# Kernel tuning notes

Hardware: AMD Instinct MI355X
Metric: run time of the kernel (lower is better)

The kernel has to match this reference:

```python
import jax, jax.numpy as jnp
import numpy as np

B, S_IN, S_CTX = 2, 4096, 512
INPUT_DIM = CTX_DIM = DIM = 1024
NUM_HEADS = 16
HEAD_DIM = DIM // NUM_HEADS
BASE = 10000.0


def rms_norm(x, scale, eps=1e-6):
    xf = x.astype(jnp.float32)
    rrms = jax.lax.rsqrt(jnp.mean(xf * xf, axis=-1, keepdims=True) + eps)
    return (xf * rrms).astype(x.dtype) * scale


def apply_rope(x, pos):
    # x: [B, N, H, D]; rotate-half RoPE over full head_dim
    d = x.shape[-1]
    inv_freq = 1.0 / (BASE ** (jnp.arange(0, d, 2, dtype=jnp.float32) / d))  # [d/2]
    ang = pos.astype(jnp.float32)[:, None] * inv_freq[None, :]  # [N, d/2]
    cos = jnp.cos(ang)[None, :, None, :]
    sin = jnp.sin(ang)[None, :, None, :]
    x1, x2 = x[..., : d // 2], x[..., d // 2 :]
    return jnp.concatenate([x1 * cos - x2 * sin, x2 * cos + x1 * sin], axis=-1).astype(x.dtype)


def setup_inputs() -> dict:
    key = jax.random.key(0)
    ks = jax.random.split(key, 8)
    std = 0.02
    return {
        "input": jax.random.normal(ks[0], (B, S_IN, INPUT_DIM), jnp.float32),
        "context": jax.random.normal(ks[1], (B, S_CTX, CTX_DIM), jnp.float32),
        "W_qkv_in": jax.random.normal(ks[2], (3 * DIM, INPUT_DIM), jnp.float32) * std,
        "b_qkv_in": jnp.zeros((3 * DIM,), jnp.float32),
        "W_qkv_ctx": jax.random.normal(ks[3], (3 * DIM, CTX_DIM), jnp.float32) * std,
        "b_qkv_ctx": jnp.zeros((3 * DIM,), jnp.float32),
        "q_scale_in": jnp.ones((DIM,), jnp.float32),
        "k_scale_in": jnp.ones((DIM,), jnp.float32),
        "q_scale_ctx": jnp.ones((DIM,), jnp.float32),
        "k_scale_ctx": jnp.ones((DIM,), jnp.float32),
        "W_out_in": jax.random.normal(ks[4], (INPUT_DIM, DIM), jnp.float32) * std,
        "b_out_in": jnp.zeros((INPUT_DIM,), jnp.float32),
        "W_out_ctx": jax.random.normal(ks[5], (CTX_DIM, DIM), jnp.float32) * std,
        "b_out_ctx": jnp.zeros((CTX_DIM,), jnp.float32),
    }


def reference(input, context, W_qkv_in, b_qkv_in, W_qkv_ctx, b_qkv_ctx,
              q_scale_in, k_scale_in, q_scale_ctx, k_scale_ctx,
              W_out_in, b_out_in, W_out_ctx, b_out_ctx):
    # dual-stream QKV projections
    qkv_i = input @ W_qkv_in.T + b_qkv_in        # [B, S_in, 3*DIM]
    qkv_c = context @ W_qkv_ctx.T + b_qkv_ctx    # [B, S_ctx, 3*DIM]
    qi, ki, vi = jnp.split(qkv_i, 3, axis=-1)
    qc, kc, vc = jnp.split(qkv_c, 3, axis=-1)
    # QK-RMSNorm over full dim (as in QKNorm(dim))
    qi, ki = rms_norm(qi, q_scale_in), rms_norm(ki, k_scale_in)
    qc, kc = rms_norm(qc, q_scale_ctx), rms_norm(kc, k_scale_ctx)
    # concat context first, then input
    q = jnp.concatenate([qc, qi], axis=1)  # [B, N, DIM]
    k = jnp.concatenate([kc, ki], axis=1)
    v = jnp.concatenate([vc, vi], axis=1)
    N = q.shape[1]
    pos = jnp.arange(N)
    # RoPE applied per head
    q = apply_rope(q.reshape(B, N, NUM_HEADS, HEAD_DIM), pos).reshape(B, N, DIM)
    k = apply_rope(k.reshape(B, N, NUM_HEADS, HEAD_DIM), pos).reshape(B, N, DIM)
    # single-head attention over full dim (faithful to source: heads flattened before q@k^T)
    scale = HEAD_DIM ** -0.5
    attn = jax.nn.softmax(jnp.einsum('bnd,bmd->bnm', q, k) * scale, axis=-1)
    out = jnp.einsum('bnm,bmd->bnd', attn, v)  # [B, N, DIM]
    s_ctx = context.shape[1]
    input_output = out[:, s_ctx:, :] @ W_out_in.T + b_out_in
    context_output = out[:, :s_ctx, :] @ W_out_ctx.T + b_out_ctx
    return (input_output, context_output)
```

## Files before the change

### kernel.cpp

```cpp
#include <hip/hip_runtime.h>
#include <stdint.h>

typedef unsigned short u16;
typedef __bf16 bf16x8 __attribute__((ext_vector_type(8)));
typedef float f32x4 __attribute__((ext_vector_type(4)));

typedef const __attribute__((address_space(1))) uint32_t* gu32p;
typedef __attribute__((address_space(3))) uint32_t* lu32p;
#define GLOAD_LDS16(g, l) \
  __builtin_amdgcn_global_load_lds((gu32p)(const void*)(g), (lu32p)(void*)(l), 16, 0, 0)

static __device__ __forceinline__ u16 f2bf(float f) {
  uint32_t u = __builtin_bit_cast(uint32_t, f);
  return (u16)((u + 0x7FFFu + ((u >> 16) & 1u)) >> 16);
}
static __device__ __forceinline__ float bf2f(u16 h) {
  uint32_t u = ((uint32_t)h) << 16;
  return __builtin_bit_cast(float, u);
}

__global__ __launch_bounds__(256) void k_conv_all(
    const float* __restrict__ s0, u16* __restrict__ d0,
    const float* __restrict__ s1, u16* __restrict__ d1,
    const float* __restrict__ s2, u16* __restrict__ d2,
    const float* __restrict__ s3, u16* __restrict__ d3,
    const float* __restrict__ s4, u16* __restrict__ d4,
    const float* __restrict__ s5, u16* __restrict__ d5) {
  int b = blockIdx.x;
  const float* src; u16* dst; long off;
  if (b < 8192)       { src = s0; dst = d0; off = (long)b * 1024; }
  else if (b < 9216)  { src = s1; dst = d1; off = (long)(b - 8192) * 1024; }
  else if (b < 12288) { src = s2; dst = d2; off = (long)(b - 9216) * 1024; }
  else if (b < 15360) { src = s3; dst = d3; off = (long)(b - 12288) * 1024; }
  else if (b < 16384) { src = s4; dst = d4; off = (long)(b - 15360) * 1024; }
  else                { src = s5; dst = d5; off = (long)(b - 16384) * 1024; }
  long i = off + threadIdx.x * 4;
  const float4 v = *(const float4*)&src[i];
  ushort4 o;
  o.x = f2bf(v.x); o.y = f2bf(v.y); o.z = f2bf(v.z); o.w = f2bf(v.w);
  *(ushort4*)&dst[i] = o;
}

__device__ __forceinline__ void gemm_bk64(const u16* __restrict__ A, const u16* __restrict__ Bt,
                                          int lda, int ldb, long row0, long col0,
                                          int kbeg, int kend, u16* smem, f32x4 acc[4][4]) {
  const int tid = threadIdx.x;
  const int l = tid & 63;
  const int w = tid >> 6;
  const int wm = w >> 1, wn = w & 1;
  const int lr = l & 15, kg = l >> 4;
  const int swz = (lr & 7) * 8;
  const int r_l = tid >> 3;
  const int ssrc = ((tid & 7) ^ (r_l & 7)) * 8;
  const u16* gA = &A[(row0 + r_l) * (long)lda + ssrc];
  const u16* gB = &Bt[(col0 + r_l) * (long)ldb + ssrc];
  u16* const ldsA = smem + w * 512;
  u16* const ldsB = smem + 8192 + w * 512;
  const int NT = (kend - kbeg) >> 6;

  {
#pragma unroll
    for (int c = 0; c < 4; ++c) {
      GLOAD_LDS16(gA + (c * 32) * (long)lda + kbeg, ldsA + c * 2048);
      GLOAD_LDS16(gB + (c * 32) * (long)ldb + kbeg, ldsB + c * 2048);
    }
  }
  asm volatile("s_waitcnt vmcnt(0)" ::: "memory");
  __builtin_amdgcn_s_barrier();
  __builtin_amdgcn_sched_barrier(0);

  for (int t = 0; t < NT; ++t) {
    const int d = (t & 1) << 14;
    const int dn = ((t + 1) & 1) << 14;
    const bool pf = (t + 1 < NT);
    const long k1 = kbeg + (long)(t + 1) * 64;
    bf16x8 af[4], bv[4];
    if (pf) {
#pragma unroll
      for (int c = 0; c < 4; ++c)
        GLOAD_LDS16(gA + (c * 32) * (long)lda + k1, ldsA + dn + c * 2048);
    }
#pragma unroll
    for (int i = 0; i < 4; ++i) {
      af[i] = *(const bf16x8*)&smem[d + (wm * 64 + i * 16 + lr) * 64 + (kg * 8 ^ swz)];
      bv[i] = *(const bf16x8*)&smem[d + 8192 + (wn * 64 + i * 16 + lr) * 64 + (kg * 8 ^ swz)];
    }
    __builtin_amdgcn_s_setprio(1);
#pragma unroll
    for (int mf = 0; mf < 4; ++mf)
#pragma unroll
      for (int nf = 0; nf < 4; ++nf)
        acc[mf][nf] = __builtin_amdgcn_mfma_f32_16x16x32_bf16(af[mf], bv[nf], acc[mf][nf], 0, 0, 0);
    __builtin_amdgcn_s_setprio(0);
    if (pf) {
#pragma unroll
      for (int c = 0; c < 4; ++c)
        GLOAD_LDS16(gB + (c * 32) * (long)ldb + k1, ldsB + dn + c * 2048);
    }
#pragma unroll
    for (int i = 0; i < 4; ++i) {
      af[i] = *(const bf16x8*)&smem[d + (wm * 64 + i * 16 + lr) * 64 + ((32 + kg * 8) ^ swz)];
      bv[i] = *(const bf16x8*)&smem[d + 8192 + (wn * 64 + i * 16 + lr) * 64 + ((32 + kg * 8) ^ swz)];
    }
    __builtin_amdgcn_s_setprio(1);
#pragma unroll
    for (int mf = 0; mf < 4; ++mf)
#pragma unroll
      for (int nf = 0; nf < 4; ++nf)
        acc[mf][nf] = __builtin_amdgcn_mfma_f32_16x16x32_bf16(af[mf], bv[nf], acc[mf][nf], 0, 0, 0);
    __builtin_amdgcn_s_setprio(0);
    asm volatile("s_waitcnt vmcnt(0)" ::: "memory");
    __builtin_amdgcn_s_barrier();
    __builtin_amdgcn_sched_barrier(0);
  }
}

#define EPI_VARS                                   \
  const int l = threadIdx.x & 63;                  \
  const int w = threadIdx.x >> 6;                  \
  const int wm = w >> 1, wn = w & 1;               \
  const int mrow = (l >> 4) * 4, ncol = l & 15;

__global__ __launch_bounds__(256, 2) void k_gemm_qkv(
    const u16* __restrict__ XIN, const u16* __restrict__ XCTX,
    const u16* __restrict__ WQI, const u16* __restrict__ WQC,
    const float* __restrict__ bqi, const float* __restrict__ bqc,
    u16* __restrict__ qb, u16* __restrict__ kb, u16* __restrict__ vt) {
  __shared__ u16 smem[32768];
  f32x4 acc[4][4] = {};
  const bool isCtx = blockIdx.x >= 64;
  const u16* X = isCtx ? XCTX : XIN;
  const u16* W = isCtx ? WQC : WQI;
  const float* bias = isCtx ? bqc : bqi;
  const int seg_start = isCtx ? 0 : 512;
  long row0 = (long)(isCtx ? blockIdx.x - 64 : blockIdx.x) * 128;
  long col0 = (long)blockIdx.y * 128;
  gemm_bk64(X, W, 1024, 1024, row0, col0, 0, 1024, smem, acc);
  EPI_VARS
#pragma unroll
  for (int mf = 0; mf < 4; ++mf)
#pragma unroll
    for (int nf = 0; nf < 4; ++nf)
#pragma unroll
      for (int r = 0; r < 4; ++r) {
        int m = (int)row0 + wm * 64 + mf * 16 + mrow + r;
        int n = (int)col0 + wn * 64 + nf * 16 + ncol;
        float v = acc[mf][nf][r] + bias[n];
        int b, s;
        if (isCtx) { b = m >> 9; s = m & 511; } else { b = m >> 12; s = m & 4095; }
        long grow = (long)b * 4608 + seg_start + s;
        if (n < 1024)      qb[grow * 1024 + n] = f2bf(v);
        else if (n < 2048) kb[grow * 1024 + (n - 1024)] = f2bf(v);
        else               vt[((long)b * 1024 + (n - 2048)) * 4608 + seg_start + s] = f2bf(v);
      }
}

__global__ __launch_bounds__(256) void k_normrope(u16* __restrict__ qb, u16* __restrict__ kb,
                                                  const float* __restrict__ qsi, const float* __restrict__ ksi,
                                                  const float* __restrict__ qsc, const float* __restrict__ ksc) {
  __shared__ float sm[4];
  const int row = blockIdx.x;
  const int which = blockIdx.y;
  const int n = row % 4608;
  u16* buf = which ? kb : qb;
  const float* scale = which ? (n < 512 ? ksc : ksi) : (n < 512 ? qsc : qsi);
  u16* rp = buf + (long)row * 1024;
  const int t = threadIdx.x;
  const int h = t >> 4;
  const int jj = (t & 15) * 2;
  const int e1 = h * 64 + jj;
  const int e2 = e1 + 32;
  uint32_t u1 = *(const uint32_t*)&rp[e1];
  uint32_t u2 = *(const uint32_t*)&rp[e2];
  float x1a = bf2f((u16)u1), x1b = bf2f((u16)(u1 >> 16));
  float x2a = bf2f((u16)u2), x2b = bf2f((u16)(u2 >> 16));
  float ss = x1a * x1a + x1b * x1b + x2a * x2a + x2b * x2b;
#pragma unroll
  for (int o = 32; o; o >>= 1) ss += __shfl_xor(ss, o, 64);
  if ((t & 63) == 0) sm[t >> 6] = ss;
  __syncthreads();
  ss = sm[0] + sm[1] + sm[2] + sm[3];
  const float rr = rsqrtf(ss * (1.0f / 1024.0f) + 1e-6f);
  float s1a = scale[e1], s1b = scale[e1 + 1], s2a = scale[e2], s2b = scale[e2 + 1];
  x1a *= rr * s1a; x1b *= rr * s1b; x2a *= rr * s2a; x2b *= rr * s2b;
  const float c = -13.287712379549449f / 32.0f;
  float fa = exp2f((float)jj * c), fb = exp2f((float)(jj + 1) * c);
  float sna, csa, snb, csb;
  sincosf((float)n * fa, &sna, &csa);
  sincosf((float)n * fb, &snb, &csb);
  u16 o1a = f2bf(x1a * csa - x2a * sna), o1b = f2bf(x1b * csb - x2b * snb);
  u16 o2a = f2bf(x2a * csa + x1a * sna), o2b = f2bf(x2b * csb + x1b * snb);
  *(uint32_t*)&rp[e1] = (uint32_t)o1a | ((uint32_t)o1b << 16);
  *(uint32_t*)&rp[e2] = (uint32_t)o2a | ((uint32_t)o2b << 16);
}

__global__ __launch_bounds__(256, 2) void k_gemm_p(const u16* __restrict__ Q, const u16* __restrict__ Kb,
                                                   u16* __restrict__ P) {
  __shared__ u16 smem[32768];
  f32x4 acc[4][4] = {};
  long row0 = (long)blockIdx.x * 128;
  long col0 = (long)blockIdx.y * 128;
  gemm_bk64(Q, Kb, 1024, 1024, row0, col0, 0, 1024, smem, acc);
  EPI_VARS
#pragma unroll
  for (int mf = 0; mf < 4; ++mf)
#pragma unroll
    for (int nf = 0; nf < 4; ++nf)
#pragma unroll
      for (int r = 0; r < 4; ++r) {
        long m = row0 + wm * 64 + mf * 16 + mrow + r;
        long n = col0 + wn * 64 + nf * 16 + ncol;
        P[m * 4608 + n] = f2bf(__expf(acc[mf][nf][r] * 0.125f));
      }
}

__global__ __launch_bounds__(256) void k_rowsum(const u16* __restrict__ P, float* __restrict__ RS) {
  __shared__ float sm[4];
  const long row = blockIdx.x;
  const uint32_t* pr = (const uint32_t*)(P + row * 4608);
  const int t = threadIdx.x;
  float s = 0.f;
#pragma unroll
  for (int i = 0; i < 9; ++i) {
    uint32_t u = pr[i * 256 + t];
    s += bf2f((u16)u) + bf2f((u16)(u >> 16));
  }
#pragma unroll
  for (int o = 32; o; o >>= 1) s += __shfl_xor(s, o, 64);
  if ((t & 63) == 0) sm[t >> 6] = s;
  __syncthreads();
  if (t == 0) RS[row] = sm[0] + sm[1] + sm[2] + sm[3];
}

__global__ __launch_bounds__(256, 2) void k_gemm_o(const u16* __restrict__ P, const u16* __restrict__ VT,
                                                   float* __restrict__ OP) {
  __shared__ u16 smem[32768];
  f32x4 acc[4][4] = {};
  long row0 = (long)blockIdx.x * 128;
  long col0 = (long)blockIdx.y * 128;
  const int kc = blockIdx.z;
  gemm_bk64(P, VT, 4608, 4608, row0, col0, kc * 2304, (kc + 1) * 2304, smem, acc);
  float* op = OP + (long)kc * 4608 * 1024;
  EPI_VARS
#pragma unroll
  for (int mf = 0; mf < 4; ++mf)
#pragma unroll
    for (int nf = 0; nf < 4; ++nf)
#pragma unroll
      for (int r = 0; r < 4; ++r) {
        long m = row0 + wm * 64 + mf * 16 + mrow + r;
        long n = col0 + wn * 64 + nf * 16 + ncol;
        op[m * 1024 + n] = acc[mf][nf][r];
      }
}

__global__ __launch_bounds__(256) void k_reduce2div(const float* __restrict__ OP,
                                                    const float* __restrict__ RS,
                                                    u16* __restrict__ AO) {
  const long st = 4608L * 1024;
  long i = ((long)blockIdx.x * 256 + threadIdx.x) * 4;
  const float inv = 1.0f / RS[i >> 10];
  float4 a = *(const float4*)&OP[i];
  float4 b = *(const float4*)&OP[i + st];
  ushort4 o;
  o.x = f2bf((a.x + b.x) * inv);
  o.y = f2bf((a.y + b.y) * inv);
  o.z = f2bf((a.z + b.z) * inv);
  o.w = f2bf((a.w + b.w) * inv);
  *(ushort4*)&AO[i] = o;
}

__global__ __launch_bounds__(256, 2) void k_gemm_out2(const u16* __restrict__ AO,
                                                      const u16* __restrict__ WOI, const u16* __restrict__ WOC,
                                                      const float* __restrict__ boi, const float* __restrict__ boc,
                                                      float* __restrict__ out) {
  __shared__ u16 smem[32768];
  f32x4 acc[4][4] = {};
  long row0 = (long)blockIdx.x * 128;
  long col0 = (long)blockIdx.y * 128;
  int b = (int)(row0 / 4608);
  int s0 = (int)(row0 % 4608);
  const bool ctx = s0 < 512;
  const u16* W = ctx ? WOC : WOI;
  const float* bias = ctx ? boc : boi;
  float* ob = ctx ? out + 8388608 + ((long)b * 512 + s0) * 1024
                  : out + ((long)b * 4096 + (s0 - 512)) * 1024;
  gemm_bk64(AO, W, 1024, 1024, row0, col0, 0, 1024, smem, acc);
  EPI_VARS
#pragma unroll
  for (int mf = 0; mf < 4; ++mf)
#pragma unroll
    for (int nf = 0; nf < 4; ++nf)
#pragma unroll
      for (int r = 0; r < 4; ++r) {
        long m = wm * 64 + mf * 16 + mrow + r;
        long n = col0 + wn * 64 + nf * 16 + ncol;
        ob[m * 1024 + n] = acc[mf][nf][r] + bias[n];
      }
}

extern "C" void kernel_launch(void* const* d_in, const int* in_sizes, int n_in,
                              void* d_out, int out_size, void* d_ws, size_t ws_size,
                              hipStream_t stream) {
  const float* input   = (const float*)d_in[0];
  const float* context = (const float*)d_in[1];
  const float* Wqi     = (const float*)d_in[2];
  const float* bqi     = (const float*)d_in[3];
  const float* Wqc     = (const float*)d_in[4];
  const float* bqc     = (const float*)d_in[5];
  const float* qsi     = (const float*)d_in[6];
  const float* ksi     = (const float*)d_in[7];
  const float* qsc     = (const float*)d_in[8];
  const float* ksc     = (const float*)d_in[9];
  const float* Woi     = (const float*)d_in[10];
  const float* boi     = (const float*)d_in[11];
  const float* Woc     = (const float*)d_in[12];
  const float* boc     = (const float*)d_in[13];
  float* out = (float*)d_out;

  uint8_t* ws = (uint8_t*)d_ws;
  u16* XIN  = (u16*)(ws + 0);
  u16* XCTX = (u16*)(ws + 16777216);
  u16* WQI  = (u16*)(ws + 18874368);
  u16* WQC  = (u16*)(ws + 25165824);
  u16* WOI  = (u16*)(ws + 31457280);
  u16* WOC  = (u16*)(ws + 33554432);
  u16* QB   = (u16*)(ws + 35651584);
  u16* KB   = (u16*)(ws + 54525952);
  u16* VT   = (u16*)(ws + 73400320);
  u16* AO   = (u16*)(ws + 92274688);
  float* S32 = (float*)(ws + 111149056);
  float* RS  = (float*)(ws + 186646528);
  u16* PB   = (u16*)(ws + 196083712);

  k_conv_all<<<dim3(17408), 256, 0, stream>>>(input, XIN, context, XCTX, Wqi, WQI,
                                              Wqc, WQC, Woi, WOI, Woc, WOC);

  k_gemm_qkv<<<dim3(72, 24), 256, 0, stream>>>(XIN, XCTX, WQI, WQC, bqi, bqc, QB, KB, VT);

  k_normrope<<<dim3(9216, 2), 256, 0, stream>>>(QB, KB, qsi, ksi, qsc, ksc);

  for (int b = 0; b < 2; ++b) {
    const u16* Qb  = QB + (long)b * 4608 * 1024;
    const u16* Kbp = KB + (long)b * 4608 * 1024;
    const u16* VTb = VT + (long)b * 1024 * 4608;
    u16* AOb = AO + (long)b * 4608 * 1024;
    k_gemm_p<<<dim3(36, 36), 256, 0, stream>>>(Qb, Kbp, PB);
    k_rowsum<<<dim3(4608), 256, 0, stream>>>(PB, RS);
    k_gemm_o<<<dim3(36, 8, 2), 256, 0, stream>>>(PB, VTb, (float*)S32);
    k_reduce2div<<<dim3(4608), 256, 0, stream>>>((const float*)S32, RS, AOb);
  }

  k_gemm_out2<<<dim3(72, 8), 256, 0, stream>>>(AO, WOI, WOC, boi, boc, out);
}
```

Baseline: 442.1 us.

## Use single-buffered high-occupancy GEMM for scores and split PV into three K-chunks

```diff
diff --git a/kernel.cpp b/kernel.cpp
--- a/kernel.cpp
+++ b/kernel.cpp
@@ -115,6 +115,48 @@
   }
 }
 
+__device__ __forceinline__ void gemm_sb64(const u16* __restrict__ A, const u16* __restrict__ Bt,
+                                          int lda, int ldb, long row0, long col0,
+                                          int kbeg, int kend, u16* smem, f32x4 acc[4][4]) {
+  const int tid = threadIdx.x;
+  const int l = tid & 63;
+  const int w = tid >> 6;
+  const int wm = w >> 1, wn = w & 1;
+  const int lr = l & 15, kg = l >> 4;
+  const int swz = (lr & 7) * 8;
+  const int r_l = tid >> 3;
+  const int ssrc = ((tid & 7) ^ (r_l & 7)) * 8;
+  const u16* gA = &A[(row0 + r_l) * (long)lda + ssrc];
+  const u16* gB = &Bt[(col0 + r_l) * (long)ldb + ssrc];
+  u16* const ldsA = smem + w * 512;
+  u16* const ldsB = smem + 8192 + w * 512;
+
+  for (int k0 = kbeg; k0 < kend; k0 += 64) {
+#pragma unroll
+    for (int c = 0; c < 4; ++c) {
+      GLOAD_LDS16(gA + (c * 32) * (long)lda + k0, ldsA + c * 2048);
+      GLOAD_LDS16(gB + (c * 32) * (long)ldb + k0, ldsB + c * 2048);
+    }
+    __syncthreads();
+    bf16x8 af[4], bv[4];
+#pragma unroll
+    for (int s = 0; s < 2; ++s) {
+      const int ko = s * 32;
+#pragma unroll
+      for (int i = 0; i < 4; ++i) {
+        af[i] = *(const bf16x8*)&smem[(wm * 64 + i * 16 + lr) * 64 + ((ko + kg * 8) ^ swz)];
+        bv[i] = *(const bf16x8*)&smem[8192 + (wn * 64 + i * 16 + lr) * 64 + ((ko + kg * 8) ^ swz)];
+      }
+#pragma unroll
+      for (int mf = 0; mf < 4; ++mf)
+#pragma unroll
+        for (int nf = 0; nf < 4; ++nf)
+          acc[mf][nf] = __builtin_amdgcn_mfma_f32_16x16x32_bf16(af[mf], bv[nf], acc[mf][nf], 0, 0, 0);
+    }
+    __syncthreads();
+  }
+}
+
 #define EPI_VARS                                   \
   const int l = threadIdx.x & 63;                  \
   const int w = threadIdx.x >> 6;                  \
@@ -194,13 +236,13 @@
   *(uint32_t*)&rp[e2] = (uint32_t)o2a | ((uint32_t)o2b << 16);
 }
 
-__global__ __launch_bounds__(256, 2) void k_gemm_p(const u16* __restrict__ Q, const u16* __restrict__ Kb,
+__global__ __launch_bounds__(256, 5) void k_gemm_p(const u16* __restrict__ Q, const u16* __restrict__ Kb,
                                                    u16* __restrict__ P) {
-  __shared__ u16 smem[32768];
+  __shared__ u16 smem[16384];
   f32x4 acc[4][4] = {};
   long row0 = (long)blockIdx.x * 128;
   long col0 = (long)blockIdx.y * 128;
-  gemm_bk64(Q, Kb, 1024, 1024, row0, col0, 0, 1024, smem, acc);
+  gemm_sb64(Q, Kb, 1024, 1024, row0, col0, 0, 1024, smem, acc);
   EPI_VARS
 #pragma unroll
   for (int mf = 0; mf < 4; ++mf)
@@ -239,7 +281,7 @@
   long row0 = (long)blockIdx.x * 128;
   long col0 = (long)blockIdx.y * 128;
   const int kc = blockIdx.z;
-  gemm_bk64(P, VT, 4608, 4608, row0, col0, kc * 2304, (kc + 1) * 2304, smem, acc);
+  gemm_bk64(P, VT, 4608, 4608, row0, col0, kc * 1536, (kc + 1) * 1536, smem, acc);
   float* op = OP + (long)kc * 4608 * 1024;
   EPI_VARS
 #pragma unroll
@@ -254,7 +296,7 @@
       }
 }
 
-__global__ __launch_bounds__(256) void k_reduce2div(const float* __restrict__ OP,
+__global__ __launch_bounds__(256) void k_reduce3div(const float* __restrict__ OP,
                                                     const float* __restrict__ RS,
                                                     u16* __restrict__ AO) {
   const long st = 4608L * 1024;
@@ -262,11 +304,12 @@
   const float inv = 1.0f / RS[i >> 10];
   float4 a = *(const float4*)&OP[i];
   float4 b = *(const float4*)&OP[i + st];
+  float4 c = *(const float4*)&OP[i + 2 * st];
   ushort4 o;
-  o.x = f2bf((a.x + b.x) * inv);
-  o.y = f2bf((a.y + b.y) * inv);
-  o.z = f2bf((a.z + b.z) * inv);
-  o.w = f2bf((a.w + b.w) * inv);
+  o.x = f2bf((a.x + b.x + c.x) * inv);
+  o.y = f2bf((a.y + b.y + c.y) * inv);
+  o.z = f2bf((a.z + b.z + c.z) * inv);
+  o.w = f2bf((a.w + b.w + c.w) * inv);
   *(ushort4*)&AO[i] = o;
 }
 
@@ -347,8 +390,8 @@
     u16* AOb = AO + (long)b * 4608 * 1024;
     k_gemm_p<<<dim3(36, 36), 256, 0, stream>>>(Qb, Kbp, PB);
     k_rowsum<<<dim3(4608), 256, 0, stream>>>(PB, RS);
-    k_gemm_o<<<dim3(36, 8, 2), 256, 0, stream>>>(PB, VTb, (float*)S32);
-    k_reduce2div<<<dim3(4608), 256, 0, stream>>>((const float*)S32, RS, AOb);
+    k_gemm_o<<<dim3(36, 8, 3), 256, 0, stream>>>(PB, VTb, (float*)S32);
+    k_reduce3div<<<dim3(4608), 256, 0, stream>>>((const float*)S32, RS, AOb);
   }
 
   k_gemm_out2<<<dim3(72, 8), 256, 0, stream>>>(AO, WOI, WOC, boi, boc, out);
```

Result: slower. 678.3 us (+53.4%).
